# Performance work log

Hardware: AMD Instinct MI355X
Metric: run time of the kernel (lower is better)

Reference implementation:

```python
import jax, jax.numpy as jnp
import numpy as np

D_MODEL = 1024
D_STATE = 16
DT_RANK = max(1, -(-D_MODEL // 16))  # ceil(d_model/16) = 64


def setup_inputs() -> dict:
    key = jax.random.key(0)
    ks = jax.random.split(key, 5)
    B, L = 4, 2048
    x = jax.random.normal(ks[0], (B, L, D_MODEL), dtype=jnp.float32)
    # A_log initialized as log(arange(1, d_state+1)) broadcast over d_model
    A_log = jnp.broadcast_to(
        jnp.log(jnp.arange(1, D_STATE + 1, dtype=jnp.float32))[None, :],
        (D_MODEL, D_STATE)).copy()
    D = jnp.ones((D_MODEL,), dtype=jnp.float32)
    # torch nn.Linear weights: [out_features, in_features]
    s1 = 1.0 / np.sqrt(D_MODEL)
    Wx = jax.random.uniform(ks[1], (DT_RANK + 2 * D_STATE, D_MODEL),
                            minval=-s1, maxval=s1, dtype=jnp.float32)
    s2 = 1.0 / np.sqrt(DT_RANK)
    dt_W = jax.random.uniform(ks[2], (D_MODEL, DT_RANK), minval=-s2, maxval=s2,
                              dtype=jnp.float32)
    dt_b = jax.random.uniform(ks[3], (D_MODEL,), minval=-s2, maxval=s2,
                              dtype=jnp.float32)
    return {"x": x, "A_log": A_log, "D": D, "Wx": Wx, "dt_W": dt_W, "dt_b": dt_b}


def reference(x, A_log, D, Wx, dt_W, dt_b):
    Bb, L, dm = x.shape
    ds = A_log.shape[1]
    dt_rank = dt_W.shape[1]
    A = -jnp.exp(A_log)                                  # [dm, ds]
    proj = jnp.einsum('bld,pd->blp', x, Wx)              # [B, L, dt_rank+2*ds]
    dt_r = proj[..., :dt_rank]
    B_in = proj[..., dt_rank:dt_rank + ds]               # [B, L, ds]
    C_in = proj[..., dt_rank + ds:]                      # [B, L, ds]
    dt = jax.nn.softplus(jnp.einsum('blr,dr->bld', dt_r, dt_W) + dt_b)  # [B, L, dm]

    def step(h, ins):
        dt_t, B_t, C_t, x_t = ins                        # [B,dm],[B,ds],[B,ds],[B,dm]
        dA = jnp.exp(dt_t[:, :, None] * A[None])         # [B, dm, ds]
        h = h * dA + (dt_t * x_t)[:, :, None] * B_t[:, None, :]
        y_t = jnp.einsum('bds,bs->bd', h, C_t)           # [B, dm]
        return h, y_t

    h0 = jnp.zeros((Bb, dm, ds), dtype=x.dtype)
    xs = (jnp.swapaxes(dt, 0, 1), jnp.swapaxes(B_in, 0, 1),
          jnp.swapaxes(C_in, 0, 1), jnp.swapaxes(x, 0, 1))
    _, ys = jax.lax.scan(step, h0, xs)                   # ys: [L, B, dm]
    y = jnp.swapaxes(ys, 0, 1)
    return y + x * D
```

## Files before the change

### kernel.cpp

```cpp
#include <hip/hip_runtime.h>
#include <math.h>

#define DM    1024
#define DS    16
#define BB    4
#define LSEQ  2048
#define LOG2E 1.44269504088896f
#define LN2   0.69314718055994f

typedef short bf16x8 __attribute__((ext_vector_type(8)));
typedef float f32x4  __attribute__((ext_vector_type(4)));

__device__ __forceinline__ unsigned short f2bf(float f) {
  unsigned u = __builtin_bit_cast(unsigned, f);
  u += 0x7FFFu + ((u >> 16) & 1u);
  return (unsigned short)(u >> 16);
}
__device__ __forceinline__ float bf2f(unsigned short h) {
  unsigned u = ((unsigned)h) << 16;
  return __builtin_bit_cast(float, u);
}

__global__ __launch_bounds__(256) void k0_pack(const float* __restrict__ Wx,
                                               const float* __restrict__ dtW,
                                               short* __restrict__ Wxh, short* __restrict__ Wxl,
                                               short* __restrict__ dtWh, short* __restrict__ dtWl) {
  const int i = (blockIdx.x * 256 + threadIdx.x) * 4;
  const float* src; short *dh, *dl; int off;
  if (i < 98304) { src = Wx;  dh = Wxh;  dl = Wxl;  off = i; }
  else           { src = dtW; dh = dtWh; dl = dtWl; off = i - 98304; }
  float4 v = *(const float4*)(src + off);
  float a[4] = {v.x, v.y, v.z, v.w};
  short h4[4], l4[4];
#pragma unroll
  for (int j = 0; j < 4; ++j) {
    unsigned short h = f2bf(a[j]);
    h4[j] = (short)h;
    l4[j] = (short)f2bf(a[j] - bf2f(h));
  }
  *(short4*)(dh + off) = make_short4(h4[0], h4[1], h4[2], h4[3]);
  *(short4*)(dl + off) = make_short4(l4[0], l4[1], l4[2], l4[3]);
}

__global__ __launch_bounds__(256) void k1_proj_mfma(const float* __restrict__ x,
                                                    const short* __restrict__ Wxh,
                                                    const short* __restrict__ Wxl,
                                                    short* __restrict__ dtrh,
                                                    short* __restrict__ dtrl,
                                                    float* __restrict__ BC) {
  __shared__ float red[4][1536];
  const int tid = threadIdx.x, w = tid >> 6, lane = tid & 63;
  const int r0 = blockIdx.x * 16;
  const int m = lane & 15, kj = (lane >> 4) * 8;
  f32x4 acc[6];
#pragma unroll
  for (int nt = 0; nt < 6; ++nt) acc[nt] = (f32x4){0.f, 0.f, 0.f, 0.f};
  const int kb = w * 256;
  for (int ks = 0; ks < 8; ++ks) {
    const int k = kb + ks * 32 + kj;
    const float* xp = x + (r0 + m) * DM + k;
    float4 a0 = *(const float4*)xp;
    float4 a1 = *(const float4*)(xp + 4);
    float av[8] = {a0.x, a0.y, a0.z, a0.w, a1.x, a1.y, a1.z, a1.w};
    bf16x8 ah, al;
#pragma unroll
    for (int j = 0; j < 8; ++j) {
      unsigned short h = f2bf(av[j]);
      ah[j] = (short)h;
      al[j] = (short)f2bf(av[j] - bf2f(h));
    }
#pragma unroll
    for (int nt = 0; nt < 6; ++nt) {
      const int bo = (nt * 16 + m) * DM + k;
      bf16x8 bh = *(const bf16x8*)(Wxh + bo);
      bf16x8 bl = *(const bf16x8*)(Wxl + bo);
      acc[nt] = __builtin_amdgcn_mfma_f32_16x16x32_bf16(ah, bh, acc[nt], 0, 0, 0);
      acc[nt] = __builtin_amdgcn_mfma_f32_16x16x32_bf16(ah, bl, acc[nt], 0, 0, 0);
      acc[nt] = __builtin_amdgcn_mfma_f32_16x16x32_bf16(al, bh, acc[nt], 0, 0, 0);
    }
  }
#pragma unroll
  for (int nt = 0; nt < 6; ++nt)
    *(f32x4*)&red[w][nt * 256 + lane * 4] = acc[nt];
  __syncthreads();
  const int p = tid;
  const int row = (p >> 6) * 4 + (p & 3), col16 = (p >> 2) & 15;
  const int grow = r0 + row;
#pragma unroll
  for (int nt = 0; nt < 6; ++nt) {
    const float v = red[0][nt * 256 + p] + red[1][nt * 256 + p] +
                    red[2][nt * 256 + p] + red[3][nt * 256 + p];
    if (nt < 4) {
      const int idx = grow * 64 + nt * 16 + col16;
      unsigned short h = f2bf(v);
      dtrh[idx] = (short)h;
      dtrl[idx] = (short)f2bf(v - bf2f(h));
    } else {
      BC[grow * 32 + (nt - 4) * 16 + col16] = v;
    }
  }
}

__global__ __launch_bounds__(256) void k2_dt_mfma(const short* __restrict__ dtrh,
                                                  const short* __restrict__ dtrl,
                                                  const short* __restrict__ dtWh,
                                                  const short* __restrict__ dtWl,
                                                  const float* __restrict__ dt_b,
                                                  float* __restrict__ out) {
  const int tid = threadIdx.x, w = tid >> 6, lane = tid & 63;
  const int r0 = blockIdx.x * 16;
  const int n0 = blockIdx.y * 256 + w * 64;
  const int m = lane & 15, quad = lane >> 4, kj = quad * 8;
  f32x4 acc[4];
#pragma unroll
  for (int nt = 0; nt < 4; ++nt) acc[nt] = (f32x4){0.f, 0.f, 0.f, 0.f};
#pragma unroll
  for (int ks = 0; ks < 2; ++ks) {
    const int k = ks * 32 + kj;
    bf16x8 ah = *(const bf16x8*)(dtrh + (r0 + m) * 64 + k);
    bf16x8 al = *(const bf16x8*)(dtrl + (r0 + m) * 64 + k);
#pragma unroll
    for (int nt = 0; nt < 4; ++nt) {
      const int bo = (n0 + nt * 16 + m) * 64 + k;
      bf16x8 bh = *(const bf16x8*)(dtWh + bo);
      bf16x8 bl = *(const bf16x8*)(dtWl + bo);
      acc[nt] = __builtin_amdgcn_mfma_f32_16x16x32_bf16(ah, bh, acc[nt], 0, 0, 0);
      acc[nt] = __builtin_amdgcn_mfma_f32_16x16x32_bf16(ah, bl, acc[nt], 0, 0, 0);
      acc[nt] = __builtin_amdgcn_mfma_f32_16x16x32_bf16(al, bh, acc[nt], 0, 0, 0);
    }
  }
#pragma unroll
  for (int nt = 0; nt < 4; ++nt) {
    const int col = n0 + nt * 16 + m;
    const float bias = dt_b[col];
#pragma unroll
    for (int i = 0; i < 4; ++i) {
      const float v = acc[nt][i] + bias;
      const float sp = fmaxf(v, 0.f) +
          LN2 * __builtin_amdgcn_logf(1.f + __builtin_amdgcn_exp2f(-LOG2E * fabsf(v)));
      out[(r0 + quad * 4 + i) * DM + col] = sp;
    }
  }
}

template <int NC>
__global__ __launch_bounds__(256) void k3_scanA(const float* __restrict__ dtb,
                                                const float* __restrict__ x,
                                                const float* __restrict__ BC,
                                                const float* __restrict__ A_log,
                                                float* __restrict__ Pws,
                                                float* __restrict__ Sws) {
  constexpr int LC = LSEQ / NC;
  const int tid = threadIdx.x, bid = blockIdx.x;
  const int dblk = bid & 3, c = (bid >> 2) % NC, b = bid / (4 * NC);
  const int d = dblk * 256 + tid;
  float Aa[DS];
#pragma unroll
  for (int q = 0; q < 4; ++q) {
    float4 v = *(const float4*)(A_log + d * DS + q * 4);
    Aa[q * 4 + 0] = -__expf(v.x) * LOG2E; Aa[q * 4 + 1] = -__expf(v.y) * LOG2E;
    Aa[q * 4 + 2] = -__expf(v.z) * LOG2E; Aa[q * 4 + 3] = -__expf(v.w) * LOG2E;
  }
  float h[DS], Pp[DS];
#pragma unroll
  for (int s = 0; s < DS; ++s) { h[s] = 0.f; Pp[s] = 1.f; }
  const int rowb = b * LSEQ + c * LC;
  float dtc = dtb[rowb * DM + d], xc = x[rowb * DM + d];
  const float* bp0 = BC + rowb * 32;
  float4 b0 = *(const float4*)bp0, b1 = *(const float4*)(bp0 + 4),
         b2 = *(const float4*)(bp0 + 8), b3 = *(const float4*)(bp0 + 12);
  for (int t = 0; t < LC; ++t) {
    const int tn = (t + 1 < LC) ? t + 1 : t;
    const int rown = rowb + tn;
    const float dtn = dtb[rown * DM + d], xn = x[rown * DM + d];
    const float* bp = BC + rown * 32;
    const float4 n0 = *(const float4*)bp, n1 = *(const float4*)(bp + 4),
                 n2 = *(const float4*)(bp + 8), n3 = *(const float4*)(bp + 12);
    float Bv[DS];
    *(float4*)&Bv[0] = b0; *(float4*)&Bv[4] = b1;
    *(float4*)&Bv[8] = b2; *(float4*)&Bv[12] = b3;
    const float u = dtc * xc;
#pragma unroll
    for (int s = 0; s < DS; ++s) {
      const float dA = __builtin_amdgcn_exp2f(dtc * Aa[s]);
      Pp[s] *= dA;
      h[s] = fmaf(h[s], dA, u * Bv[s]);
    }
    dtc = dtn; xc = xn; b0 = n0; b1 = n1; b2 = n2; b3 = n3;
  }
  const int base = ((b * NC + c) * DM + d) * DS;
#pragma unroll
  for (int q = 0; q < 4; ++q) {
    *(float4*)(Pws + base + q * 4) = make_float4(Pp[q*4], Pp[q*4+1], Pp[q*4+2], Pp[q*4+3]);
    *(float4*)(Sws + base + q * 4) = make_float4(h[q*4], h[q*4+1], h[q*4+2], h[q*4+3]);
  }
}

template <int NC>
__global__ __launch_bounds__(256) void k3_comb(float* __restrict__ PH,
                                               const float* __restrict__ Sws) {
  const int t = blockIdx.x * 256 + threadIdx.x;
  const int b = t >> 14, dsi = t & 16383;
  const int cb0 = b * NC;
  float h = 0.f;
  for (int cb = 0; cb < NC; cb += 8) {
    float p[8], s[8];
#pragma unroll
    for (int j = 0; j < 8; ++j) {
      const int idx = ((cb0 + cb + j) << 14) + dsi;
      p[j] = PH[idx]; s[j] = Sws[idx];
    }
#pragma unroll
    for (int j = 0; j < 8; ++j) {
      const int idx = ((cb0 + cb + j) << 14) + dsi;
      PH[idx] = h;
      h = fmaf(p[j], h, s[j]);
    }
  }
}

template <int NC>
__global__ __launch_bounds__(256) void k3_scanC(float* __restrict__ io,
                                                const float* __restrict__ x,
                                                const float* __restrict__ BC,
                                                const float* __restrict__ A_log,
                                                const float* __restrict__ Dvec,
                                                const float* __restrict__ Hin) {
  constexpr int LC = LSEQ / NC;
  const int tid = threadIdx.x, bid = blockIdx.x;
  const int dblk = bid & 3, c = (bid >> 2) % NC, b = bid / (4 * NC);
  const int d = dblk * 256 + tid;
  float Aa[DS];
#pragma unroll
  for (int q = 0; q < 4; ++q) {
    float4 v = *(const float4*)(A_log + d * DS + q * 4);
    Aa[q * 4 + 0] = -__expf(v.x) * LOG2E; Aa[q * 4 + 1] = -__expf(v.y) * LOG2E;
    Aa[q * 4 + 2] = -__expf(v.z) * LOG2E; Aa[q * 4 + 3] = -__expf(v.w) * LOG2E;
  }
  float h[DS];
  const int base = ((b * NC + c) * DM + d) * DS;
#pragma unroll
  for (int q = 0; q < 4; ++q)
    *(float4*)&h[q * 4] = *(const float4*)(Hin + base + q * 4);
  const float Dv = Dvec[d];
  const int rowb = b * LSEQ + c * LC;
  float dtc = io[rowb * DM + d], xc = x[rowb * DM + d];
  const float* p0 = BC + rowb * 32;
  float4 b0 = *(const float4*)p0,      b1 = *(const float4*)(p0 + 4),
         b2 = *(const float4*)(p0 + 8), b3 = *(const float4*)(p0 + 12),
         c0 = *(const float4*)(p0 + 16), c1 = *(const float4*)(p0 + 20),
         c2 = *(const float4*)(p0 + 24), c3 = *(const float4*)(p0 + 28);
  for (int t = 0; t < LC; ++t) {
    const int tn = (t + 1 < LC) ? t + 1 : t;
    const int rown = rowb + tn;
    const float dtn = io[rown * DM + d], xn = x[rown * DM + d];
    const float* bp = BC + rown * 32;
    const float4 nb0 = *(const float4*)bp,        nb1 = *(const float4*)(bp + 4),
                 nb2 = *(const float4*)(bp + 8),  nb3 = *(const float4*)(bp + 12),
                 nc0 = *(const float4*)(bp + 16), nc1 = *(const float4*)(bp + 20),
                 nc2 = *(const float4*)(bp + 24), nc3 = *(const float4*)(bp + 28);
    float Bv[DS], Cv[DS];
    *(float4*)&Bv[0] = b0; *(float4*)&Bv[4] = b1;
    *(float4*)&Bv[8] = b2; *(float4*)&Bv[12] = b3;
    *(float4*)&Cv[0] = c0; *(float4*)&Cv[4] = c1;
    *(float4*)&Cv[8] = c2; *(float4*)&Cv[12] = c3;
    const float u = dtc * xc;
    float y = 0.f;
#pragma unroll
    for (int s = 0; s < DS; ++s) {
      const float dA = __builtin_amdgcn_exp2f(dtc * Aa[s]);
      h[s] = fmaf(h[s], dA, u * Bv[s]);
      y = fmaf(h[s], Cv[s], y);
    }
    io[(rowb + t) * DM + d] = fmaf(xc, Dv, y);
    dtc = dtn; xc = xn;
    b0 = nb0; b1 = nb1; b2 = nb2; b3 = nb3;
    c0 = nc0; c1 = nc1; c2 = nc2; c3 = nc3;
  }
}

extern "C" void kernel_launch(void* const* d_in, const int* in_sizes, int n_in,
                              void* d_out, int out_size, void* d_ws, size_t ws_size,
                              hipStream_t stream) {
  const float* x     = (const float*)d_in[0];
  const float* A_log = (const float*)d_in[1];
  const float* Dvec  = (const float*)d_in[2];
  const float* Wx    = (const float*)d_in[3];
  const float* dt_W  = (const float*)d_in[4];
  const float* dt_b  = (const float*)d_in[5];
  float* out = (float*)d_out;
  float* ws  = (float*)d_ws;

  short* Wxh  = (short*)ws;
  short* Wxl  = Wxh + 98304;
  short* dtWh = Wxl + 98304;
  short* dtWl = dtWh + 65536;
  short* dtrh = dtWl + 65536;
  short* dtrl = dtrh + 524288;
  float* BC   = ws + 688128;
  float* P    = BC + 262144;

  k0_pack<<<160, 256, 0, stream>>>(Wx, dt_W, Wxh, Wxl, dtWh, dtWl);
  k1_proj_mfma<<<512, 256, 0, stream>>>(x, Wxh, Wxl, dtrh, dtrl, BC);
  k2_dt_mfma<<<dim3(512, 4), 256, 0, stream>>>(dtrh, dtrl, dtWh, dtWl, dt_b, out);

  if (ws_size >= (size_t)(950272 + 2 * 64 * 65536) * 4) {
    constexpr int NC = 64;
    float* S = P + NC * 65536;
    k3_scanA<NC><<<BB * NC * 4, 256, 0, stream>>>(out, x, BC, A_log, P, S);
    k3_comb<NC><<<256, 256, 0, stream>>>(P, S);
    k3_scanC<NC><<<BB * NC * 4, 256, 0, stream>>>(out, x, BC, A_log, Dvec, P);
  } else {
    constexpr int NC = 32;
    float* S = P + NC * 65536;
    k3_scanA<NC><<<BB * NC * 4, 256, 0, stream>>>(out, x, BC, A_log, P, S);
    k3_comb<NC><<<256, 256, 0, stream>>>(P, S);
    k3_scanC<NC><<<BB * NC * 4, 256, 0, stream>>>(out, x, BC, A_log, Dvec, P);
  }
}
```

Before: 210.7 us.

## Stage B/C rows in LDS and prefetch dt/x in groups of eight in scan kernels

Both chunked-scan kernels now copy their chunk's B (and C) projection rows into shared memory once per block, then read them from LDS as broadcasts instead of issuing per-timestep global float4 loads. The dt and x loads are also grouped eight timesteps at a time with a one-group-ahead prefetch, giving more memory-level parallelism than the old single-step prefetch. This costs more registers and shared memory per block, which may lower occupancy. In scanC, io is still overwritten in place while a later group of dt values is being prefetched, but the prefetch only reads rows ahead of the ones written, so this stays safe.

Result: slower. 219.1 us (+4.0%).

```diff
diff --git a/kernel.cpp b/kernel.cpp
--- a/kernel.cpp
+++ b/kernel.cpp
@@ -151,9 +151,18 @@
                                                 float* __restrict__ Pws,
                                                 float* __restrict__ Sws) {
   constexpr int LC = LSEQ / NC;
+  constexpr int G = 8, NG = LC / G;
+  __shared__ float Bs[LC][16];
   const int tid = threadIdx.x, bid = blockIdx.x;
   const int dblk = bid & 3, c = (bid >> 2) % NC, b = bid / (4 * NC);
   const int d = dblk * 256 + tid;
+  const int rowb = b * LSEQ + c * LC;
+
+  for (int i = tid; i < LC * 4; i += 256) {
+    const int r = i >> 2, q = i & 3;
+    *(float4*)&Bs[r][q * 4] = *(const float4*)(BC + (rowb + r) * 32 + q * 4);
+  }
+
   float Aa[DS];
 #pragma unroll
   for (int q = 0; q < 4; ++q) {
@@ -164,30 +173,43 @@
   float h[DS], Pp[DS];
 #pragma unroll
   for (int s = 0; s < DS; ++s) { h[s] = 0.f; Pp[s] = 1.f; }
-  const int rowb = b * LSEQ + c * LC;
-  float dtc = dtb[rowb * DM + d], xc = x[rowb * DM + d];
-  const float* bp0 = BC + rowb * 32;
-  float4 b0 = *(const float4*)bp0, b1 = *(const float4*)(bp0 + 4),
-         b2 = *(const float4*)(bp0 + 8), b3 = *(const float4*)(bp0 + 12);
-  for (int t = 0; t < LC; ++t) {
-    const int tn = (t + 1 < LC) ? t + 1 : t;
-    const int rown = rowb + tn;
-    const float dtn = dtb[rown * DM + d], xn = x[rown * DM + d];
-    const float* bp = BC + rown * 32;
-    const float4 n0 = *(const float4*)bp, n1 = *(const float4*)(bp + 4),
-                 n2 = *(const float4*)(bp + 8), n3 = *(const float4*)(bp + 12);
-    float Bv[DS];
-    *(float4*)&Bv[0] = b0; *(float4*)&Bv[4] = b1;
-    *(float4*)&Bv[8] = b2; *(float4*)&Bv[12] = b3;
-    const float u = dtc * xc;
-#pragma unroll
-    for (int s = 0; s < DS; ++s) {
-      const float dA = __builtin_amdgcn_exp2f(dtc * Aa[s]);
-      Pp[s] *= dA;
-      h[s] = fmaf(h[s], dA, u * Bv[s]);
-    }
-    dtc = dtn; xc = xn; b0 = n0; b1 = n1; b2 = n2; b3 = n3;
-  }
+
+  float dtc[G], xc[G];
+#pragma unroll
+  for (int j = 0; j < G; ++j) {
+    dtc[j] = dtb[(rowb + j) * DM + d];
+    xc[j]  = x[(rowb + j) * DM + d];
+  }
+  __syncthreads();
+
+#pragma unroll 1
+  for (int g = 0; g < NG; ++g) {
+    float dtn[G], xn[G];
+    const int nb = rowb + ((g + 1 < NG) ? (g + 1) : g) * G;
+#pragma unroll
+    for (int j = 0; j < G; ++j) {
+      dtn[j] = dtb[(nb + j) * DM + d];
+      xn[j]  = x[(nb + j) * DM + d];
+    }
+#pragma unroll
+    for (int j = 0; j < G; ++j) {
+      const int t = g * G + j;
+      float Bv[DS];
+#pragma unroll
+      for (int q = 0; q < 4; ++q)
+        *(float4*)&Bv[q * 4] = *(const float4*)&Bs[t][q * 4];
+      const float u = dtc[j] * xc[j];
+#pragma unroll
+      for (int s = 0; s < DS; ++s) {
+        const float dA = __builtin_amdgcn_exp2f(dtc[j] * Aa[s]);
+        Pp[s] *= dA;
+        h[s] = fmaf(h[s], dA, u * Bv[s]);
+      }
+    }
+#pragma unroll
+    for (int j = 0; j < G; ++j) { dtc[j] = dtn[j]; xc[j] = xn[j]; }
+  }
+
   const int base = ((b * NC + c) * DM + d) * DS;
 #pragma unroll
   for (int q = 0; q < 4; ++q) {
@@ -203,6 +225,7 @@
   const int b = t >> 14, dsi = t & 16383;
   const int cb0 = b * NC;
   float h = 0.f;
+#pragma unroll 1
   for (int cb = 0; cb < NC; cb += 8) {
     float p[8], s[8];
 #pragma unroll
@@ -227,9 +250,18 @@
                                                 const float* __restrict__ Dvec,
                                                 const float* __restrict__ Hin) {
   constexpr int LC = LSEQ / NC;
+  constexpr int G = 8, NG = LC / G;
+  __shared__ float BCs[LC][32];
   const int tid = threadIdx.x, bid = blockIdx.x;
   const int dblk = bid & 3, c = (bid >> 2) % NC, b = bid / (4 * NC);
   const int d = dblk * 256 + tid;
+  const int rowb = b * LSEQ + c * LC;
+
+  for (int i = tid; i < LC * 8; i += 256) {
+    const int r = i >> 3, q = i & 7;
+    *(float4*)&BCs[r][q * 4] = *(const float4*)(BC + (rowb + r) * 32 + q * 4);
+  }
+
   float Aa[DS];
 #pragma unroll
   for (int q = 0; q < 4; ++q) {
@@ -243,39 +275,45 @@
   for (int q = 0; q < 4; ++q)
     *(float4*)&h[q * 4] = *(const float4*)(Hin + base + q * 4);
   const float Dv = Dvec[d];
-  const int rowb = b * LSEQ + c * LC;
-  float dtc = io[rowb * DM + d], xc = x[rowb * DM + d];
-  const float* p0 = BC + rowb * 32;
-  float4 b0 = *(const float4*)p0,      b1 = *(const float4*)(p0 + 4),
-         b2 = *(const float4*)(p0 + 8), b3 = *(const float4*)(p0 + 12),
-         c0 = *(const float4*)(p0 + 16), c1 = *(const float4*)(p0 + 20),
-         c2 = *(const float4*)(p0 + 24), c3 = *(const float4*)(p0 + 28);
-  for (int t = 0; t < LC; ++t) {
-    const int tn = (t + 1 < LC) ? t + 1 : t;
-    const int rown = rowb + tn;
-    const float dtn = io[rown * DM + d], xn = x[rown * DM + d];
-    const float* bp = BC + rown * 32;
-    const float4 nb0 = *(const float4*)bp,        nb1 = *(const float4*)(bp + 4),
-                 nb2 = *(const float4*)(bp + 8),  nb3 = *(const float4*)(bp + 12),
-                 nc0 = *(const float4*)(bp + 16), nc1 = *(const float4*)(bp + 20),
-                 nc2 = *(const float4*)(bp + 24), nc3 = *(const float4*)(bp + 28);
-    float Bv[DS], Cv[DS];
-    *(float4*)&Bv[0] = b0; *(float4*)&Bv[4] = b1;
-    *(float4*)&Bv[8] = b2; *(float4*)&Bv[12] = b3;
-    *(float4*)&Cv[0] = c0; *(float4*)&Cv[4] = c1;
-    *(float4*)&Cv[8] = c2; *(float4*)&Cv[12] = c3;
-    const float u = dtc * xc;
-    float y = 0.f;
-#pragma unroll
-    for (int s = 0; s < DS; ++s) {
-      const float dA = __builtin_amdgcn_exp2f(dtc * Aa[s]);
-      h[s] = fmaf(h[s], dA, u * Bv[s]);
-      y = fmaf(h[s], Cv[s], y);
-    }
-    io[(rowb + t) * DM + d] = fmaf(xc, Dv, y);
-    dtc = dtn; xc = xn;
-    b0 = nb0; b1 = nb1; b2 = nb2; b3 = nb3;
-    c0 = nc0; c1 = nc1; c2 = nc2; c3 = nc3;
+
+  float dtc[G], xc[G];
+#pragma unroll
+  for (int j = 0; j < G; ++j) {
+    dtc[j] = io[(rowb + j) * DM + d];
+    xc[j]  = x[(rowb + j) * DM + d];
+  }
+  __syncthreads();
+
+#pragma unroll 1
+  for (int g = 0; g < NG; ++g) {
+    float dtn[G], xn[G];
+    const int nb = rowb + ((g + 1 < NG) ? (g + 1) : g) * G;
+#pragma unroll
+    for (int j = 0; j < G; ++j) {
+      dtn[j] = io[(nb + j) * DM + d];
+      xn[j]  = x[(nb + j) * DM + d];
+    }
+#pragma unroll
+    for (int j = 0; j < G; ++j) {
+      const int t = g * G + j;
+      float Bv[DS], Cv[DS];
+#pragma unroll
+      for (int q = 0; q < 4; ++q) {
+        *(float4*)&Bv[q * 4] = *(const float4*)&BCs[t][q * 4];
+        *(float4*)&Cv[q * 4] = *(const float4*)&BCs[t][16 + q * 4];
+      }
+      const float u = dtc[j] * xc[j];
+      float y = 0.f;
+#pragma unroll
+      for (int s = 0; s < DS; ++s) {
+        const float dA = __builtin_amdgcn_exp2f(dtc[j] * Aa[s]);
+        h[s] = fmaf(h[s], dA, u * Bv[s]);
+        y = fmaf(h[s], Cv[s], y);
+      }
+      io[(rowb + t) * DM + d] = fmaf(xc[j], Dv, y);
+    }
+#pragma unroll
+    for (int j = 0; j < G; ++j) { dtc[j] = dtn[j]; xc[j] = xn[j]; }
   }
 }
 
```
